# Optimization experiments

Measured on AMD Instinct MI355X. Metric: run time of the kernel, lower is better.

## Reference

```python
import jax, jax.numpy as jnp
import numpy as np
import math

B, T, D, H = 16, 256, 1024, 1024
SEG = 16              # segment_len
S = T // SEG          # number of cached segment slots (max_cached_segments=None)
SCALE = 1.0 / math.sqrt(H)


def _ln(x, g, b, eps=1e-5):
    m = jnp.mean(x, -1, keepdims=True)
    v = jnp.mean((x - m) ** 2, -1, keepdims=True)
    return (x - m) * jax.lax.rsqrt(v + eps) * g + b


def _lstm_cell(inp, h, c, Wih, Whh, bih, bhh):
    z = inp @ Wih.T + bih + h @ Whh.T + bhh
    i, f, g, o = jnp.split(z, 4, axis=-1)  # torch LSTMCell gate order i,f,g,o
    c2 = jax.nn.sigmoid(f) * c + jax.nn.sigmoid(i) * jnp.tanh(g)
    return jax.nn.sigmoid(o) * jnp.tanh(c2), c2


def setup_inputs() -> dict:
    key = jax.random.key(0)
    it = iter(jax.random.split(key, 40))

    def un(shape, fan):
        lim = 1.0 / np.sqrt(fan)
        return jax.random.uniform(next(it), shape, jnp.float32, -lim, lim)

    inp = {}
    inp['x'] = jax.random.normal(next(it), (B, T, D), jnp.float32)
    inp['W_ip'] = un((D, D), D); inp['b_ip'] = un((D,), D)
    inp['g_ip'] = jnp.ones((D,), jnp.float32); inp['be_ip'] = jnp.zeros((D,), jnp.float32)
    inp['W_ih0'] = un((4 * H, D), H); inp['W_hh0'] = un((4 * H, H), H)
    inp['b_ih0'] = un((4 * H,), H); inp['b_hh0'] = un((4 * H,), H)
    inp['W_ih1'] = un((4 * H, H), H); inp['W_hh1'] = un((4 * H, H), H)
    inp['b_ih1'] = un((4 * H,), H); inp['b_hh1'] = un((4 * H,), H)
    inp['Wq'] = un((H, H), H); inp['Wk'] = un((H, H), H); inp['Wv'] = un((H, H), H)
    inp['Wg1'] = un((H, 3 * H), 3 * H); inp['bg1'] = un((H,), 3 * H)
    inp['Wg2'] = un((H, H), H); inp['bg2'] = un((H,), H)
    inp['Wo'] = un((H, H), H); inp['bo'] = un((H,), H)
    inp['Wf'] = un((H, 2 * H), 2 * H); inp['bf'] = un((H,), 2 * H)
    inp['g_f'] = jnp.ones((H,), jnp.float32); inp['be_f'] = jnp.zeros((H,), jnp.float32)
    return inp


def reference(x, W_ip, b_ip, g_ip, be_ip,
              W_ih0, W_hh0, b_ih0, b_hh0,
              W_ih1, W_hh1, b_ih1, b_hh1,
              Wq, Wk, Wv, Wg1, bg1, Wg2, bg2, Wo, bo,
              Wf, bf, g_f, be_f):
    # input_proj (eval mode: dropout = identity)
    xp = jax.nn.relu(_ln(x @ W_ip.T + b_ip, g_ip, be_ip))      # [B,T,D]
    xseg = xp.transpose(1, 0, 2).reshape(S, SEG, B, D)          # [S,SEG,B,D]

    def seg_body(carry, xs):
        h0, c0, h1, c1, kbank, vbank = carry
        x_s, s = xs                                             # x_s:[SEG,B,D], s = #cached segments
        valid = jnp.arange(S) < s

        def step(inner, xt):
            h0, c0, h1, c1, seg_sum = inner
            h0, c0 = _lstm_cell(xt, h0, c0, W_ih0, W_hh0, b_ih0, b_hh0)
            h1, c1 = _lstm_cell(h0, h1, c1, W_ih1, W_hh1, b_ih1, b_hh1)
            # SegmentMemoryRetriever, cache_mode='gated_residual'
            q = h1 @ Wq.T
            scores = jnp.einsum('bh,sbh->bs', q, kbank) * SCALE
            scores = jnp.where(valid[None, :], scores, -1e9)
            attn = jax.nn.softmax(scores, axis=-1)
            retrieved = jnp.einsum('bs,sbh->bh', attn, vbank)
            gi = jnp.concatenate([h1, retrieved, h1 - retrieved], -1)
            gate = jax.nn.sigmoid(jax.nn.relu(gi @ Wg1.T + bg1) @ Wg2.T + bg2)
            out = (gate * h1 + (1.0 - gate) * retrieved) @ Wo.T + bo
            ret = jnp.where(s > 0, out, jnp.zeros_like(out))    # empty cache -> zero retrieval
            enh = jax.nn.relu(_ln(jnp.concatenate([h1, ret], -1) @ Wf.T + bf, g_f, be_f))
            return (h0, c0, h1, c1, seg_sum + h1), enh

        init = (h0, c0, h1, c1, jnp.zeros_like(h1))
        (h0, c0, h1, c1, seg_sum), enh = jax.lax.scan(step, init, x_s)
        # append segment to cache; keys/values projected once (linear, equivalent)
        kbank = kbank.at[s].set((seg_sum / SEG) @ Wk.T)         # context = segment mean (use_segment_context)
        vbank = vbank.at[s].set(h1 @ Wv.T)                      # memory = last top hidden of segment
        return (h0, c0, h1, c1, kbank, vbank), enh

    z = jnp.zeros((B, H), x.dtype)
    bank = jnp.zeros((S, B, H), x.dtype)
    carry0 = (z, z, z, z, bank, bank)
    _, enh = jax.lax.scan(seg_body, carry0, (xseg, jnp.arange(S)))
    return enh.reshape(T, B, H).transpose(1, 0, 2)              # sequence_output [B,T,H]
```

## Files before the change

### kernel.cpp

```cpp
#include <hip/hip_runtime.h>
#include <hip/hip_bf16.h>
#include <math.h>

#define B_ 16
#define T_ 256
#define D_ 1024
#define H_ 1024
#define S_ 16
#define SCALE_ (1.0f/32.0f)

typedef __attribute__((ext_vector_type(8))) short short8v;
typedef __attribute__((ext_vector_type(4))) float f32x4;

__device__ __forceinline__ float sigm(float x) { return 1.f / (1.f + expf(-x)); }

__device__ __forceinline__ ushort f2b(float v) {
  __hip_bfloat16 h = __float2bfloat16(v);
  return *reinterpret_cast<ushort*>(&h);
}
__device__ __forceinline__ float b2f(ushort u) {
  union { unsigned u32; float f; } x; x.u32 = ((unsigned)u) << 16; return x.f;
}

__device__ __forceinline__ void glds16(const void* g, void* l) {
  __builtin_amdgcn_global_load_lds((const __attribute__((address_space(1))) void*)g,
                                   (__attribute__((address_space(3))) void*)l, 16, 0, 0);
}

__device__ __forceinline__ void waitflags64(const int* f, int lane) {
  for (;;) {
    int v = __hip_atomic_load(f + lane, __ATOMIC_RELAXED, __HIP_MEMORY_SCOPE_AGENT);
    if (__all(v != 0)) return;
    __builtin_amdgcn_s_sleep(1);
  }
}

__device__ __forceinline__ void publish_pair(ushort* base, int tid, ushort hb) {
  unsigned hi = (unsigned)__shfl_down((int)hb, 1);
  if (!(tid & 1)) {
    unsigned word = (unsigned)hb | (hi << 16);
    __hip_atomic_exchange((unsigned*)base, word,
                          __ATOMIC_RELAXED, __HIP_MEMORY_SCOPE_AGENT);
  }
}

__device__ __forceinline__ float block_sum256(float v) {
  __shared__ float lds[4];
  #pragma unroll
  for (int off = 32; off; off >>= 1) v += __shfl_down(v, off);
  int w = threadIdx.x >> 6;
  if ((threadIdx.x & 63) == 0) lds[w] = v;
  __syncthreads();
  float r = lds[0] + lds[1] + lds[2] + lds[3];
  __syncthreads();
  return r;
}

#define NJOBS 12
struct CvtJobs {
  const float* src[NJOBS];
  ushort* dst[NJOBS];
  int cum[NJOBS + 1];
};

__global__ __launch_bounds__(256)
void cvt_all(CvtJobs J)
{
  int i = blockIdx.x * 256 + threadIdx.x;
  if (i >= J.cum[NJOBS]) return;
  int j = 0;
  #pragma unroll
  for (int k = 1; k < NJOBS; ++k) j += (i >= J.cum[k]) ? 1 : 0;
  int idx = i - J.cum[j];
  float4 v = ((const float4*)J.src[j])[idx];
  ushort4 o; o.x = f2b(v.x); o.y = f2b(v.y); o.z = f2b(v.z); o.w = f2b(v.w);
  ((ushort4*)J.dst[j])[idx] = o;
}

__global__ __launch_bounds__(256)
void tr_cvt(const float* __restrict__ src, ushort* __restrict__ dst)
{
  __shared__ float tile[64][65];
  const int bx = blockIdx.x, by = blockIdx.y;
  const int tx = threadIdx.x & 15, ty = threadIdx.x >> 4;
  #pragma unroll
  for (int p = 0; p < 4; ++p) {
    int r = p * 16 + ty;
    float4 v = *(const float4*)(src + (size_t)(by * 64 + r) * 1024 + bx * 64 + tx * 4);
    tile[r][tx*4+0] = v.x; tile[r][tx*4+1] = v.y;
    tile[r][tx*4+2] = v.z; tile[r][tx*4+3] = v.w;
  }
  __syncthreads();
  #pragma unroll
  for (int p = 0; p < 4; ++p) {
    int c = p * 16 + ty;
    ushort4 o;
    o.x = f2b(tile[tx*4+0][c]); o.y = f2b(tile[tx*4+1][c]);
    o.z = f2b(tile[tx*4+2][c]); o.w = f2b(tile[tx*4+3][c]);
    *(ushort4*)(dst + (size_t)(bx * 64 + c) * 1024 + by * 64 + tx * 4) = o;
  }
}

__global__ __launch_bounds__(256)
void wg1_fold(const float* __restrict__ Wg1, ushort* __restrict__ dst)
{
  int n = blockIdx.x;
  int c4 = threadIdx.x * 4;
  const float* row = Wg1 + (size_t)n * 3072;
  float4 a = *(const float4*)(row + c4);
  float4 b = *(const float4*)(row + 1024 + c4);
  float4 c = *(const float4*)(row + 2048 + c4);
  ushort4 h, r;
  h.x = f2b(a.x + c.x); h.y = f2b(a.y + c.y);
  h.z = f2b(a.z + c.z); h.w = f2b(a.w + c.w);
  r.x = f2b(b.x - c.x); r.y = f2b(b.y - c.y);
  r.z = f2b(b.z - c.z); r.w = f2b(b.w - c.w);
  *(ushort4*)(dst + (size_t)n * 2048 + c4) = h;
  *(ushort4*)(dst + (size_t)n * 2048 + 1024 + c4) = r;
}

template<int ACT, int REMAP>
__global__ __launch_bounds__(256)
void gemm_bf16(const ushort* __restrict__ A, const ushort* __restrict__ W,
               const float* __restrict__ bias,
               float* __restrict__ Cf, ushort* __restrict__ Cb,
               int M, int N, int K, float ascale, int ldc,
               const ushort* __restrict__ Hx, const ushort* __restrict__ Rxb,
               const ushort* __restrict__ W2, float ascale2, int msplit)
{
  __shared__ char As[16384];
  __shared__ char Bs[16384];
  const int tid = threadIdx.x;
  const int w = tid >> 6, l = tid & 63;
  const int m0 = blockIdx.y * 128, n0 = blockIdx.x * 128;
  const ushort* __restrict__ Wp = (m0 < msplit) ? W : W2;
  const float asc = (m0 < msplit) ? ascale : ascale2;
  const int wm = w >> 1, wn = w & 1;
  const int srow = l >> 3;
  const int sbyte = ((l & 7) * 16) ^ (srow << 4);
  f32x4 acc[4][4];
  #pragma unroll
  for (int i = 0; i < 4; ++i)
    #pragma unroll
    for (int j = 0; j < 4; ++j) acc[i][j] = (f32x4){0.f, 0.f, 0.f, 0.f};

  for (int k0 = 0; k0 < K; k0 += 64) {
    __syncthreads();
    #pragma unroll
    for (int c = 0; c < 4; ++c) {
      int ca = w * 4 + c;
      int r = ca * 8 + srow;
      glds16((const char*)A + (((size_t)(m0 + r) * K + k0) << 1) + sbyte, As + ca * 1024);
      glds16((const char*)Wp + (((size_t)(n0 + r) * K + k0) << 1) + sbyte, Bs + ca * 1024);
    }
    __syncthreads();
    #pragma unroll
    for (int ks = 0; ks < 2; ++ks) {
      short8v a[4], b[4];
      int qb = ks * 64 + (l >> 4) * 16;
      #pragma unroll
      for (int i = 0; i < 4; ++i) {
        int ra = wm * 64 + i * 16 + (l & 15);
        a[i] = *(const short8v*)(As + ra * 128 + (qb ^ ((ra & 7) << 4)));
        int rb = wn * 64 + i * 16 + (l & 15);
        b[i] = *(const short8v*)(Bs + rb * 128 + (qb ^ ((rb & 7) << 4)));
      }
      #pragma unroll
      for (int i = 0; i < 4; ++i)
        #pragma unroll
        for (int j = 0; j < 4; ++j)
          acc[i][j] = __builtin_amdgcn_mfma_f32_16x16x32_bf16(a[i], b[j], acc[i][j], 0, 0, 0);
    }
  }
  #pragma unroll
  for (int i = 0; i < 4; ++i) {
    #pragma unroll
    for (int j = 0; j < 4; ++j) {
      int n = n0 + wn * 64 + j * 16 + (l & 15);
      float bv = bias ? bias[n] : 0.f;
      #pragma unroll
      for (int q = 0; q < 4; ++q) {
        int m = m0 + wm * 64 + i * 16 + (l >> 4) * 4 + q;
        float v = acc[i][j][q] * asc + bv;
        if (ACT == 1) v = fmaxf(v, 0.f);
        if (ACT == 3) {
          float gte = sigm(v);
          float h = b2f(Hx[(size_t)m * 1024 + n]);
          float r = b2f(Rxb[(size_t)m * 2048 + n]);
          v = gte * h + (1.f - gte) * r;
        }
        if (ACT == 4) v = (m >= 256) ? v : 0.f;
        size_t off = REMAP ? ((size_t)((m & 255) * 16 + (m >> 8)) * ldc + n)
                           : ((size_t)m * ldc + n);
        if (Cf) Cf[off] = v;
        if (Cb) Cb[off] = f2b(v);
      }
    }
  }
}

__global__ __launch_bounds__(256)
void ln_relu_bf16(const ushort* __restrict__ X, const float* __restrict__ g,
                  const float* __restrict__ be, ushort* __restrict__ out)
{
  size_t row = blockIdx.x;
  int tid = threadIdx.x;
  ushort4 u = *(const ushort4*)(X + row * 1024 + tid * 4);
  float vx = b2f(u.x), vy = b2f(u.y), vz = b2f(u.z), vw = b2f(u.w);
  float s = block_sum256(vx + vy + vz + vw);
  float mean = s * (1.f / 1024.f);
  float dx = vx - mean, dy = vy - mean, dz = vz - mean, dw = vw - mean;
  float ss = block_sum256(dx*dx + dy*dy + dz*dz + dw*dw);
  float r = rsqrtf(ss * (1.f / 1024.f) + 1e-5f);
  int c4 = tid * 4;
  ushort4 o;
  o.x = f2b(fmaxf(dx * r * g[c4+0] + be[c4+0], 0.f));
  o.y = f2b(fmaxf(dy * r * g[c4+1] + be[c4+1], 0.f));
  o.z = f2b(fmaxf(dz * r * g[c4+2] + be[c4+2], 0.f));
  o.w = f2b(fmaxf(dw * r * g[c4+3] + be[c4+3], 0.f));
  *(ushort4*)(out + row * 1024 + c4) = o;
}

__global__ __launch_bounds__(256)
void ln_relu_final(const float* __restrict__ F, const float* __restrict__ g,
                   const float* __restrict__ be, float* __restrict__ out)
{
  int row = blockIdx.x;
  int t = row >> 4, b = row & 15;
  const float4* p = (const float4*)(F + (size_t)row * 1024);
  int tid = threadIdx.x;
  float4 v = p[tid];
  float s = block_sum256(v.x + v.y + v.z + v.w);
  float mean = s * (1.f / 1024.f);
  float dx = v.x - mean, dy = v.y - mean, dz = v.z - mean, dw = v.w - mean;
  float ss = block_sum256(dx*dx + dy*dy + dz*dz + dw*dw);
  float r = rsqrtf(ss * (1.f / 1024.f) + 1e-5f);
  int c4 = tid * 4;
  float4 o;
  o.x = fmaxf(dx * r * g[c4+0] + be[c4+0], 0.f);
  o.y = fmaxf(dy * r * g[c4+1] + be[c4+1], 0.f);
  o.z = fmaxf(dz * r * g[c4+2] + be[c4+2], 0.f);
  o.w = fmaxf(dw * r * g[c4+3] + be[c4+3], 0.f);
  ((float4*)(out + ((size_t)b * T_ + t) * 1024))[tid] = o;
}

__global__ __launch_bounds__(512)
void lstm_persistent(const ushort* __restrict__ Z0T,
                     const ushort* __restrict__ whh0,
                     const float* __restrict__ bhh0,
                     const ushort* __restrict__ wih1,
                     const ushort* __restrict__ whh1,
                     const float* __restrict__ bih1,
                     const float* __restrict__ bhh1,
                     ushort* __restrict__ HP,
                     ushort* __restrict__ H1B,
                     const ushort* __restrict__ ZP,
                     float* __restrict__ KSUM,
                     int* flag0,
                     int* flag1)
{
  __shared__ char Ah[65536];
  __shared__ float zs[8][16][16];
  __builtin_amdgcn_fence(__ATOMIC_ACQUIRE, "agent");
  const int tid = threadIdx.x, w = tid >> 6, l = tid & 63;
  const int lm = l & 15, lq = l >> 4;
  const int g = w & 3, kh = w >> 2;
  const int jb = blockIdx.x & 63;
  const int j0 = jb * 16;
  const int eb = tid >> 4, ej = tid & 15, jf = j0 + ej;
  float creg = 0.f;
  float br[4];

  if (blockIdx.x < 64) {
    short8v wreg[16];
    {
      const int n = g * 1024 + j0 + lm;
      const ushort* wb = whh0 + (size_t)n * 1024 + kh * 512 + lq * 8;
      #pragma unroll
      for (int ks = 0; ks < 16; ++ks) wreg[ks] = *(const short8v*)(wb + ks * 32);
    }
    if (tid < 256) {
      #pragma unroll
      for (int gg = 0; gg < 4; ++gg) br[gg] = bhh0[gg * 1024 + jf];
    }
    for (int t = 0; t < T_; ++t) {
      float z0v[4];
      if (tid < 256) {
        const ushort* zp = Z0T + ((size_t)t * 16 + eb) * 4096 + jf;
        #pragma unroll
        for (int gg = 0; gg < 4; ++gg) z0v[gg] = b2f(zp[gg * 1024]);
      }
      if (t > 0) {
        if (w == 0) waitflags64(flag0 + (size_t)t * 64, l);
        __syncthreads();
      }
      const ushort* hin = HP + (size_t)t * 16384;
      #pragma unroll
      for (int it = 0; it < 4; ++it) {
        int g1k = w * 4 + it;
        int kc = g1k * 4 + lq;
        int m = lm ^ (kc & 15);
        glds16(hin + (size_t)m * 1024 + kc * 8, Ah + g1k * 1024);
      }
      __syncthreads();
      {
        f32x4 a0 = {0.f,0.f,0.f,0.f}, a1 = {0.f,0.f,0.f,0.f};
        #pragma unroll
        for (int ks = 0; ks < 16; ks += 2) {
          int kc0 = kh * 64 + ks * 4 + lq;
          int kc1 = kc0 + 4;
          short8v f0 = *(const short8v*)(Ah + kc0 * 256 + ((lm ^ (kc0 & 15)) << 4));
          short8v f1 = *(const short8v*)(Ah + kc1 * 256 + ((lm ^ (kc1 & 15)) << 4));
          a0 = __builtin_amdgcn_mfma_f32_16x16x32_bf16(f0, wreg[ks],     a0, 0, 0, 0);
          a1 = __builtin_amdgcn_mfma_f32_16x16x32_bf16(f1, wreg[ks + 1], a1, 0, 0, 0);
        }
        #pragma unroll
        for (int q = 0; q < 4; ++q) zs[w][lq * 4 + q][lm] = a0[q] + a1[q];
      }
      __syncthreads();
      if (tid < 256) {
        float zi = zs[0][eb][ej] + zs[4][eb][ej] + z0v[0] + br[0];
        float zf = zs[1][eb][ej] + zs[5][eb][ej] + z0v[1] + br[1];
        float zg = zs[2][eb][ej] + zs[6][eb][ej] + z0v[2] + br[2];
        float zo = zs[3][eb][ej] + zs[7][eb][ej] + z0v[3] + br[3];
        float cp = sigm(zf) * creg + sigm(zi) * tanhf(zg);
        creg = cp;
        ushort hb = f2b(sigm(zo) * tanhf(cp));
        publish_pair(HP + (size_t)(t + 1) * 16384 + eb * 1024 + jf, tid, hb);
      }
      __syncthreads();
      if (tid == 0)
        __hip_atomic_store(flag0 + (size_t)(t + 1) * 64 + jb, 1,
                           __ATOMIC_RELAXED, __HIP_MEMORY_SCOPE_AGENT);
    }
  } else {
    short8v wreg[32];
    {
      const int n = g * 1024 + j0 + lm;
      const ushort* wb = (kh ? whh1 : wih1) + (size_t)n * 1024 + lq * 8;
      #pragma unroll
      for (int ks = 0; ks < 32; ++ks) wreg[ks] = *(const short8v*)(wb + ks * 32);
    }
    if (tid < 256) {
      #pragma unroll
      for (int gg = 0; gg < 4; ++gg)
        br[gg] = bih1[gg * 1024 + jf] + bhh1[gg * 1024 + jf];
    }
    float ksr = 0.f;
    for (int t = 0; t < T_; ++t) {
      if (w == 0) waitflags64(flag0 + (size_t)(t + 1) * 64, l);
      __syncthreads();
      const ushort* h0n = HP + (size_t)(t + 1) * 16384;
      #pragma unroll
      for (int it = 0; it < 4; ++it) {
        int g1k = w * 4 + it;
        int kc = g1k * 4 + lq;
        int m = lm ^ (kc & 15);
        glds16(h0n + (size_t)m * 1024 + kc * 8, Ah + g1k * 1024);
      }
      if (w == 1 && t > 0) waitflags64(flag1 + (size_t)(t - 1) * 64, l);
      __syncthreads();
      const ushort* h1p = (t > 0) ? (H1B + (size_t)(t - 1) * 16384) : ZP;
      #pragma unroll
      for (int it = 0; it < 4; ++it) {
        int g1k = 32 + w * 4 + it;
        int kc = g1k * 4 + lq;
        int m = lm ^ (kc & 15);
        glds16(h1p + (size_t)m * 1024 + (kc - 128) * 8, Ah + g1k * 1024);
      }
      __syncthreads();
      {
        f32x4 a0 = {0.f,0.f,0.f,0.f}, a1 = {0.f,0.f,0.f,0.f};
        #pragma unroll
        for (int ks = 0; ks < 32; ks += 2) {
          int kc0 = kh * 128 + ks * 4 + lq;
          int kc1 = kc0 + 4;
          short8v f0 = *(const short8v*)(Ah + kc0 * 256 + ((lm ^ (kc0 & 15)) << 4));
          short8v f1 = *(const short8v*)(Ah + kc1 * 256 + ((lm ^ (kc1 & 15)) << 4));
          a0 = __builtin_amdgcn_mfma_f32_16x16x32_bf16(f0, wreg[ks],     a0, 0, 0, 0);
          a1 = __builtin_amdgcn_mfma_f32_16x16x32_bf16(f1, wreg[ks + 1], a1, 0, 0, 0);
        }
        #pragma unroll
        for (int q = 0; q < 4; ++q) zs[w][lq * 4 + q][lm] = a0[q] + a1[q];
      }
      __syncthreads();
      if (tid < 256) {
        float zi = zs[0][eb][ej] + zs[4][eb][ej] + br[0];
        float zf = zs[1][eb][ej] + zs[5][eb][ej] + br[1];
        float zg = zs[2][eb][ej] + zs[6][eb][ej] + br[2];
        float zo = zs[3][eb][ej] + zs[7][eb][ej] + br[3];
        float cp = sigm(zf) * creg + sigm(zi) * tanhf(zg);
        creg = cp;
        float hv = sigm(zo) * tanhf(cp);
        ksr += hv;
        publish_pair(H1B + (size_t)t * 16384 + eb * 1024 + jf, tid, f2b(hv));
        if ((t & 15) == 15) {
          KSUM[((size_t)(t >> 4) * 16 + eb) * 1024 + jf] = ksr;
          ksr = 0.f;
        }
      }
      __syncthreads();
      if (tid == 0)
        __hip_atomic_store(flag1 + (size_t)t * 64 + jb, 1,
                           __ATOMIC_RELAXED, __HIP_MEMORY_SCOPE_AGENT);
    }
  }
}

__global__ __launch_bounds__(256)
void prep_banks(const float* __restrict__ KSUM, ushort* __restrict__ KSB,
                const ushort* __restrict__ H1B)
{
  int r = blockIdx.x;
  int c4 = threadIdx.x * 4;
  float4 v = *(const float4*)(KSUM + (size_t)r * 1024 + c4);
  ushort4 o; o.x = f2b(v.x); o.y = f2b(v.y); o.z = f2b(v.z); o.w = f2b(v.w);
  *(ushort4*)(KSB + (size_t)r * 1024 + c4) = o;
  int src = (r >> 4) * 256 + 240 + (r & 15);
  *(ushort4*)(KSB + (size_t)(256 + r) * 1024 + c4) =
      *(const ushort4*)(H1B + (size_t)src * 1024 + c4);
}

__global__ __launch_bounds__(256)
void attn_rh(const ushort* __restrict__ H1B, const ushort* __restrict__ KKb,
             const ushort* __restrict__ vbank, ushort* __restrict__ RHB)
{
  int row = blockIdx.x;
  int t = row >> 4, b = row & 15;
  int si = t >> 4;
  int tid = threadIdx.x, lane = tid & 63, w = tid >> 6;
  __shared__ float sc[16];
  float4 accv = {0.f, 0.f, 0.f, 0.f};
  if (si > 0) {
    const ushort* q = H1B + (size_t)row * 1024;
    for (int s = w; s < si; s += 4) {
      const ushort* kk = KKb + ((size_t)s * 16 + b) * 1024;
      float p = 0.f;
      for (int k = lane; k < 1024; k += 64) p += b2f(q[k]) * b2f(kk[k]);
      #pragma unroll
      for (int off = 32; off; off >>= 1) p += __shfl_down(p, off);
      if (lane == 0) sc[s] = p * SCALE_;
    }
    __syncthreads();
    float mx = -1e30f;
    for (int s = 0; s < si; ++s) mx = fmaxf(mx, sc[s]);
    float den = 0.f;
    for (int s = 0; s < si; ++s) den += expf(sc[s] - mx);
    float inv = 1.f / den;
    for (int s = 0; s < si; ++s) {
      float a = expf(sc[s] - mx) * inv;
      ushort4 vv = *(const ushort4*)(vbank + ((size_t)s * 16 + b) * 1024 + tid * 4);
      accv.x += a * b2f(vv.x); accv.y += a * b2f(vv.y);
      accv.z += a * b2f(vv.z); accv.w += a * b2f(vv.w);
    }
  }
  size_t r = row;
  int c4 = tid * 4;
  ushort4 h4 = *(const ushort4*)(H1B + r * 1024 + c4);
  *(ushort4*)(RHB + r * 2048 + c4) = h4;
  ushort4 rb; rb.x = f2b(accv.x); rb.y = f2b(accv.y);
  rb.z = f2b(accv.z); rb.w = f2b(accv.w);
  *(ushort4*)(RHB + r * 2048 + 1024 + c4) = rb;
}

extern "C" void kernel_launch(void* const* d_in, const int* in_sizes, int n_in,
                              void* d_out, int out_size, void* d_ws, size_t ws_size,
                              hipStream_t stream) {
  const float* x     = (const float*)d_in[0];
  const float* W_ip  = (const float*)d_in[1];
  const float* b_ip  = (const float*)d_in[2];
  const float* g_ip  = (const float*)d_in[3];
  const float* be_ip = (const float*)d_in[4];
  const float* W_ih0 = (const float*)d_in[5];
  const float* W_hh0 = (const float*)d_in[6];
  const float* b_ih0 = (const float*)d_in[7];
  const float* b_hh0 = (const float*)d_in[8];
  const float* W_ih1 = (const float*)d_in[9];
  const float* W_hh1 = (const float*)d_in[10];
  const float* b_ih1 = (const float*)d_in[11];
  const float* b_hh1 = (const float*)d_in[12];
  const float* Wq    = (const float*)d_in[13];
  const float* Wk    = (const float*)d_in[14];
  const float* Wv    = (const float*)d_in[15];
  const float* Wg1   = (const float*)d_in[16];
  const float* bg1   = (const float*)d_in[17];
  const float* Wg2   = (const float*)d_in[18];
  const float* bg2   = (const float*)d_in[19];
  const float* Wo    = (const float*)d_in[20];
  const float* bo    = (const float*)d_in[21];
  const float* Wf    = (const float*)d_in[22];
  const float* bff   = (const float*)d_in[23];
  const float* g_f   = (const float*)d_in[24];
  const float* be_f  = (const float*)d_in[25];
  float* out = (float*)d_out;
  char* ws = (char*)d_ws;
  const size_t MB = (size_t)1 << 20;
  const size_t KB = (size_t)1 << 10;

  ushort* WB = (ushort*)(ws);
  ushort* wipB  = WB;
  ushort* wih0B = WB + 1*1048576;
  ushort* whh0B = WB + 5*1048576;
  ushort* wih1B = WB + 9*1048576;
  ushort* whh1B = WB + 13*1048576;
  ushort* wqTB  = WB + 17*1048576;
  ushort* wkB   = WB + 18*1048576;
  ushort* wvB   = WB + 19*1048576;
  ushort* wg1F  = WB + 20*1048576;
  ushort* wg2B  = WB + 23*1048576;
  ushort* woB   = WB + 24*1048576;
  ushort* wfB   = WB + 25*1048576;

  ushort* XB   = (ushort*)(ws + 54 * MB);
  ushort* XPP  = (ushort*)(ws + 62 * MB);
  char*   SCR  = ws + 78 * MB;
  ushort* Z0T  = (ushort*)SCR;
  ushort* RHB  = (ushort*)SCR;
  ushort* G1B  = (ushort*)(SCR + 16 * MB);
  ushort* MIXB = (ushort*)(SCR + 24 * MB);
  float*  FB   = (float*)(SCR + 32 * MB);
  ushort* H1B  = (ushort*)(ws + 126 * MB);
  ushort* HP   = (ushort*)(ws + 134 * MB);
  char*   ST   = ws + 150 * MB;
  int*    flag0 = (int*)(ST);
  int*    flag1 = (int*)(ST + 68 * KB);
  const ushort* ZPc = (const ushort*)(ST + 132 * KB);
  float*  KSUM = (float*)(ST + 192 * KB);
  ushort* KSB  = (ushort*)(ST + 1216 * KB);
  ushort* KBb  = (ushort*)(ST + 2240 * KB);
  ushort* VBb  = KBb + 256 * 1024;
  ushort* KKb  = (ushort*)(ST + 3264 * KB);

  hipMemsetAsync(ST, 0, 164 * KB, stream);
  hipMemsetAsync(HP, 0, 32 * KB, stream);

  dim3 blk(256);
  {
    CvtJobs J;
    const float* srcs[NJOBS] = { x, W_ip, W_ih0, W_hh0, W_ih1, W_hh1,
                                 Wk, Wv, Wg2, Wo, Wf, nullptr };
    ushort* dsts[NJOBS] = { XB, wipB, wih0B, whh0B, wih1B, whh1B,
                            wkB, wvB, wg2B, woB, wfB, nullptr };
    int n4[NJOBS] = { 1048576, 262144, 1048576, 1048576, 1048576, 1048576,
                      262144, 262144, 262144, 262144, 524288, 0 };
    int c = 0;
    for (int j = 0; j < NJOBS; ++j) {
      J.src[j] = srcs[j] ? srcs[j] : x;
      J.dst[j] = dsts[j] ? dsts[j] : XB;
      J.cum[j] = c;
      c += n4[j];
    }
    J.cum[NJOBS] = c;
    cvt_all<<<dim3((c + 255) / 256), blk, 0, stream>>>(J);
  }
  tr_cvt<<<dim3(16, 16), blk, 0, stream>>>(Wq, wqTB);
  wg1_fold<<<1024, blk, 0, stream>>>(Wg1, wg1F);

  const int BIG = 1 << 30;
  gemm_bf16<0,0><<<dim3(1024/128, 4096/128), blk, 0, stream>>>(
      XB, wipB, b_ip, nullptr, XPP, 4096, 1024, 1024, 1.f, 1024,
      nullptr, nullptr, wipB, 1.f, BIG);
  ln_relu_bf16<<<4096, blk, 0, stream>>>(XPP, g_ip, be_ip, XB);
  gemm_bf16<0,1><<<dim3(4096/128, 4096/128), blk, 0, stream>>>(
      XB, wih0B, b_ih0, nullptr, Z0T, 4096, 4096, 1024, 1.f, 4096,
      nullptr, nullptr, wih0B, 1.f, BIG);
  {
    void* kargs[] = {
      (void*)&Z0T, (void*)&whh0B, (void*)&b_hh0,
      (void*)&wih1B, (void*)&whh1B, (void*)&b_ih1, (void*)&b_hh1,
      (void*)&HP, (void*)&H1B, (void*)&ZPc, (void*)&KSUM,
      (void*)&flag0, (void*)&flag1
    };
    hipLaunchCooperativeKernel((const void*)lstm_persistent,
                               dim3(128), dim3(512), kargs, 0, stream);
  }
  prep_banks<<<256, blk, 0, stream>>>(KSUM, KSB, H1B);
  gemm_bf16<0,0><<<dim3(1024/128, 512/128), blk, 0, stream>>>(
      KSB, wkB, nullptr, nullptr, KBb, 512, 1024, 1024, 1.f/16.f, 1024,
      nullptr, nullptr, wvB, 1.f, 256);
  gemm_bf16<0,0><<<dim3(1024/128, 256/128), blk, 0, stream>>>(
      KBb, wqTB, nullptr, nullptr, KKb, 256, 1024, 1024, 1.f, 1024,
      nullptr, nullptr, wqTB, 1.f, BIG);
  attn_rh<<<4096, blk, 0, stream>>>(H1B, KKb, VBb, RHB);
  gemm_bf16<1,0><<<dim3(1024/128, 4096/128), blk, 0, stream>>>(
      RHB, wg1F, bg1, nullptr, G1B, 4096, 1024, 2048, 1.f, 1024,
      nullptr, nullptr, wg1F, 1.f, BIG);
  gemm_bf16<3,0><<<dim3(1024/128, 4096/128), blk, 0, stream>>>(
      G1B, wg2B, bg2, nullptr, MIXB, 4096, 1024, 1024, 1.f, 1024,
      H1B, RHB + 1024, wg2B, 1.f, BIG);
  gemm_bf16<4,0><<<dim3(1024/128, 4096/128), blk, 0, stream>>>(
      MIXB, woB, bo, nullptr, RHB + 1024, 4096, 1024, 1024, 1.f, 2048,
      nullptr, nullptr, woB, 1.f, BIG);
  gemm_bf16<0,0><<<dim3(1024/128, 4096/128), blk, 0, stream>>>(
      RHB, wfB, bff, FB, nullptr, 4096, 1024, 2048, 1.f, 1024,
      nullptr, nullptr, wfB, 1.f, BIG);
  ln_relu_final<<<4096, blk, 0, stream>>>(FB, g_f, be_f, out);
}
```

Measured before the change: 1.358 ms.

## Fuse layer-0 input projection into persistent LSTM recurrence kernel

Removes the separate large GEMM that precomputed layer-0 input gate pre-activations. The persistent LSTM blocks now hold W_ih0 slices in registers and multiply the LN-ReLU output (written time-major) inside each timestep. The recurrence also no longer reads the precomputed Z0T buffer. In exchange, each serial timestep on the 64 layer-0 blocks does twice the MFMA work and stages twice the shared data. Register pressure doubles for the weight slices, which may lengthen the critical recurrent path.

```diff
diff --git a/kernel.cpp b/kernel.cpp
--- a/kernel.cpp
+++ b/kernel.cpp
@@ -200,12 +200,12 @@
 }
 
 __global__ __launch_bounds__(256)
-void ln_relu_bf16(const ushort* __restrict__ X, const float* __restrict__ g,
-                  const float* __restrict__ be, ushort* __restrict__ out)
-{
-  size_t row = blockIdx.x;
+void ln_relu_remap(const ushort* __restrict__ X, const float* __restrict__ g,
+                   const float* __restrict__ be, ushort* __restrict__ out)
+{
+  int m = blockIdx.x;
   int tid = threadIdx.x;
-  ushort4 u = *(const ushort4*)(X + row * 1024 + tid * 4);
+  ushort4 u = *(const ushort4*)(X + (size_t)m * 1024 + tid * 4);
   float vx = b2f(u.x), vy = b2f(u.y), vz = b2f(u.z), vw = b2f(u.w);
   float s = block_sum256(vx + vy + vz + vw);
   float mean = s * (1.f / 1024.f);
@@ -218,7 +218,8 @@
   o.y = f2b(fmaxf(dy * r * g[c4+1] + be[c4+1], 0.f));
   o.z = f2b(fmaxf(dz * r * g[c4+2] + be[c4+2], 0.f));
   o.w = f2b(fmaxf(dw * r * g[c4+3] + be[c4+3], 0.f));
-  *(ushort4*)(out + row * 1024 + c4) = o;
+  size_t orow = (size_t)((m & 255) * 16 + (m >> 8));
+  *(ushort4*)(out + orow * 1024 + c4) = o;
 }
 
 __global__ __launch_bounds__(256)
@@ -245,8 +246,10 @@
 }
 
 __global__ __launch_bounds__(512)
-void lstm_persistent(const ushort* __restrict__ Z0T,
+void lstm_persistent(const ushort* __restrict__ XPT,
+                     const ushort* __restrict__ wih0,
                      const ushort* __restrict__ whh0,
+                     const float* __restrict__ bih0,
                      const float* __restrict__ bhh0,
                      const ushort* __restrict__ wih1,
                      const ushort* __restrict__ whh1,
@@ -272,35 +275,41 @@
   float br[4];
 
   if (blockIdx.x < 64) {
-    short8v wreg[16];
+    short8v wreg[16], wreg2[16];
     {
       const int n = g * 1024 + j0 + lm;
-      const ushort* wb = whh0 + (size_t)n * 1024 + kh * 512 + lq * 8;
-      #pragma unroll
-      for (int ks = 0; ks < 16; ++ks) wreg[ks] = *(const short8v*)(wb + ks * 32);
+      const ushort* wb  = whh0 + (size_t)n * 1024 + kh * 512 + lq * 8;
+      const ushort* wb2 = wih0 + (size_t)n * 1024 + kh * 512 + lq * 8;
+      #pragma unroll
+      for (int ks = 0; ks < 16; ++ks) wreg[ks]  = *(const short8v*)(wb  + ks * 32);
+      #pragma unroll
+      for (int ks = 0; ks < 16; ++ks) wreg2[ks] = *(const short8v*)(wb2 + ks * 32);
     }
     if (tid < 256) {
       #pragma unroll
-      for (int gg = 0; gg < 4; ++gg) br[gg] = bhh0[gg * 1024 + jf];
+      for (int gg = 0; gg < 4; ++gg)
+        br[gg] = bhh0[gg * 1024 + jf] + bih0[gg * 1024 + jf];
     }
     for (int t = 0; t < T_; ++t) {
-      float z0v[4];
-      if (tid < 256) {
-        const ushort* zp = Z0T + ((size_t)t * 16 + eb) * 4096 + jf;
-        #pragma unroll
-        for (int gg = 0; gg < 4; ++gg) z0v[gg] = b2f(zp[gg * 1024]);
-      }
       if (t > 0) {
         if (w == 0) waitflags64(flag0 + (size_t)t * 64, l);
         __syncthreads();
       }
       const ushort* hin = HP + (size_t)t * 16384;
+      const ushort* xin = XPT + (size_t)t * 16384;
       #pragma unroll
       for (int it = 0; it < 4; ++it) {
         int g1k = w * 4 + it;
         int kc = g1k * 4 + lq;
         int m = lm ^ (kc & 15);
         glds16(hin + (size_t)m * 1024 + kc * 8, Ah + g1k * 1024);
+      }
+      #pragma unroll
+      for (int it = 0; it < 4; ++it) {
+        int g1k = 32 + w * 4 + it;
+        int kc = g1k * 4 + lq;
+        int m = lm ^ (kc & 15);
+        glds16(xin + (size_t)m * 1024 + (kc - 128) * 8, Ah + g1k * 1024);
       }
       __syncthreads();
       {
@@ -315,14 +324,23 @@
           a1 = __builtin_amdgcn_mfma_f32_16x16x32_bf16(f1, wreg[ks + 1], a1, 0, 0, 0);
         }
         #pragma unroll
+        for (int ks = 0; ks < 16; ks += 2) {
+          int kc0 = 128 + kh * 64 + ks * 4 + lq;
+          int kc1 = kc0 + 4;
+          short8v f0 = *(const short8v*)(Ah + kc0 * 256 + ((lm ^ (kc0 & 15)) << 4));
+          short8v f1 = *(const short8v*)(Ah + kc1 * 256 + ((lm ^ (kc1 & 15)) << 4));
+          a0 = __builtin_amdgcn_mfma_f32_16x16x32_bf16(f0, wreg2[ks],     a0, 0, 0, 0);
+          a1 = __builtin_amdgcn_mfma_f32_16x16x32_bf16(f1, wreg2[ks + 1], a1, 0, 0, 0);
+        }
+        #pragma unroll
         for (int q = 0; q < 4; ++q) zs[w][lq * 4 + q][lm] = a0[q] + a1[q];
       }
       __syncthreads();
       if (tid < 256) {
-        float zi = zs[0][eb][ej] + zs[4][eb][ej] + z0v[0] + br[0];
-        float zf = zs[1][eb][ej] + zs[5][eb][ej] + z0v[1] + br[1];
-        float zg = zs[2][eb][ej] + zs[6][eb][ej] + z0v[2] + br[2];
-        float zo = zs[3][eb][ej] + zs[7][eb][ej] + z0v[3] + br[3];
+        float zi = zs[0][eb][ej] + zs[4][eb][ej] + br[0];
+        float zf = zs[1][eb][ej] + zs[5][eb][ej] + br[1];
+        float zg = zs[2][eb][ej] + zs[6][eb][ej] + br[2];
+        float zo = zs[3][eb][ej] + zs[7][eb][ej] + br[3];
         float cp = sigm(zf) * creg + sigm(zi) * tanhf(zg);
         creg = cp;
         ushort hb = f2b(sigm(zo) * tanhf(cp));
@@ -514,7 +532,7 @@
   ushort* XB   = (ushort*)(ws + 54 * MB);
   ushort* XPP  = (ushort*)(ws + 62 * MB);
   char*   SCR  = ws + 78 * MB;
-  ushort* Z0T  = (ushort*)SCR;
+  ushort* XPT  = (ushort*)SCR;
   ushort* RHB  = (ushort*)SCR;
   ushort* G1B  = (ushort*)(SCR + 16 * MB);
   ushort* MIXB = (ushort*)(SCR + 24 * MB);
@@ -560,13 +578,10 @@
   gemm_bf16<0,0><<<dim3(1024/128, 4096/128), blk, 0, stream>>>(
       XB, wipB, b_ip, nullptr, XPP, 4096, 1024, 1024, 1.f, 1024,
       nullptr, nullptr, wipB, 1.f, BIG);
-  ln_relu_bf16<<<4096, blk, 0, stream>>>(XPP, g_ip, be_ip, XB);
-  gemm_bf16<0,1><<<dim3(4096/128, 4096/128), blk, 0, stream>>>(
-      XB, wih0B, b_ih0, nullptr, Z0T, 4096, 4096, 1024, 1.f, 4096,
-      nullptr, nullptr, wih0B, 1.f, BIG);
+  ln_relu_remap<<<4096, blk, 0, stream>>>(XPP, g_ip, be_ip, XPT);
   {
     void* kargs[] = {
-      (void*)&Z0T, (void*)&whh0B, (void*)&b_hh0,
+      (void*)&XPT, (void*)&wih0B, (void*)&whh0B, (void*)&b_ih0, (void*)&b_hh0,
       (void*)&wih1B, (void*)&whh1B, (void*)&b_ih1, (void*)&b_hh1,
       (void*)&HP, (void*)&H1B, (void*)&ZPc, (void*)&KSUM,
       (void*)&flag0, (void*)&flag1
```

New measurement: 1.612 ms. 18.7% more time.
